# Optimization experiments

Hardware: AMD Instinct MI355X
Metric: run time of the kernel (lower is better)

The kernel has to match this reference:

```python
import jax, jax.numpy as jnp
import numpy as np

N = 50000       # nodes
E = 1_600_000   # edges (avg degree 32)
NFEAT = 256
NHID = 128
NCLASS = 128    # must equal NHID for the gated skip connection to type-check


def setup_inputs() -> dict:
    key = jax.random.key(0)
    ks = jax.random.split(key, 16)
    g = 0.02  # xavier gain used in the module
    inp = {
        "x": jax.random.normal(ks[0], (N, NFEAT), dtype=jnp.float32),
        "row": jax.random.randint(ks[1], (E,), 0, N, dtype=jnp.int32),
        "col": jax.random.randint(ks[2], (E,), 0, N, dtype=jnp.int32),
        # GatedSkipConnection params (shared across the three skip calls)
        "W_sc": jax.random.normal(ks[3], (NFEAT, NHID), dtype=jnp.float32) * 0.05,
        "W_ci": jax.random.normal(ks[4], (NHID, NHID), dtype=jnp.float32) * 0.05,
        "b_ci": jnp.zeros((NHID,), dtype=jnp.float32),
        "W_co": jax.random.normal(ks[5], (NHID, NHID), dtype=jnp.float32) * 0.05,
        "b_co": jnp.zeros((NHID,), dtype=jnp.float32),
        # GraphSAGE layer weights: [2*in, out], bias [1, out] (init to 0 per module)
        "W0": jax.random.normal(ks[6], (2 * NFEAT, NHID), dtype=jnp.float32) * g,
        "b0": jnp.zeros((1, NHID), dtype=jnp.float32),
        "W1": jax.random.normal(ks[7], (2 * NHID, NHID), dtype=jnp.float32) * g,
        "b1": jnp.zeros((1, NHID), dtype=jnp.float32),
        "W2": jax.random.normal(ks[8], (2 * NHID, NCLASS), dtype=jnp.float32) * g,
        "b2": jnp.zeros((1, NCLASS), dtype=jnp.float32),
        # fc0: Linear(nhid, nclass)
        "Wf": jax.random.normal(ks[9], (NHID, NCLASS), dtype=jnp.float32) * 0.05,
        "bf": jnp.zeros((NCLASS,), dtype=jnp.float32),
    }
    return inp


def _sage(x, row, col, inv_deg, W, b):
    # adj @ x : sum source features x[col] into destination rows `row`
    agg = jax.ops.segment_sum(x[col], row, num_segments=N)  # [N, d]
    agg = agg * inv_deg[:, None]                            # degree normalization
    support = jnp.concatenate([x, agg], axis=1)             # [N, 2d]
    return support @ W + b


def _gsc(in_x, out_x, W_sc, W_ci, b_ci, W_co, b_co):
    in_x = in_x @ W_sc if in_x.shape[1] != out_x.shape[1] else in_x
    z = jax.nn.sigmoid(in_x @ W_ci + b_ci + out_x @ W_co + b_co)
    return z * out_x + (1.0 - z) * in_x


def reference(x, row, col, W_sc, W_ci, b_ci, W_co, b_co,
              W0, b0, W1, b1, W2, b2, Wf, bf):
    deg = jax.ops.segment_sum(jnp.ones((E,), x.dtype), row, num_segments=N)
    inv_deg = 1.0 / jnp.maximum(deg, 1.0)  # guard isolated nodes

    residual = x
    o1 = _sage(x, row, col, inv_deg, W0, b0)
    o3 = jax.nn.relu(_gsc(residual, o1, W_sc, W_ci, b_ci, W_co, b_co))
    o4 = _sage(o3, row, col, inv_deg, W1, b1)
    o6 = jax.nn.relu(_gsc(residual, o4, W_sc, W_ci, b_ci, W_co, b_co))
    o7 = _sage(o6, row, col, inv_deg, W2, b2)
    o8 = _gsc(residual, o7, W_sc, W_ci, b_ci, W_co, b_co)
    return o8 @ Wf + bf
```

## Files before the change

### kernel.cpp

```cpp
#include <hip/hip_runtime.h>
#include <hip/hip_bf16.h>
#include <hip/hip_fp16.h>
#include <math.h>

#define NN 50000
#define EE 1600000
#define NFEAT 256
#define NHID 128
#define RNG 6250
#define NPASS 8

typedef _Float16 f16;
typedef _Float16 f16x8 __attribute__((ext_vector_type(8)));
typedef _Float16 f16x4 __attribute__((ext_vector_type(4)));
typedef float f32x4 __attribute__((ext_vector_type(4)));

__global__ void k_zero_i32(int* __restrict__ p, int n) {
    int i = blockIdx.x * 256 + threadIdx.x;
    if (i < n) p[i] = 0;
}

__global__ void k_slot(const int* __restrict__ row, int* __restrict__ cnt,
                       int* __restrict__ eslot, int e) {
    int i = blockIdx.x * 256 + threadIdx.x;
    if (i < e) eslot[i] = atomicAdd(&cnt[row[i]], 1);
}

__global__ void k_scan1(const int* __restrict__ deg, int* __restrict__ bsum, int n) {
    __shared__ int s[256];
    int t = threadIdx.x;
    int i = blockIdx.x * 256 + t;
    s[t] = (i < n) ? deg[i] : 0;
    __syncthreads();
    for (int off = 128; off > 0; off >>= 1) {
        if (t < off) s[t] += s[t + off];
        __syncthreads();
    }
    if (t == 0) bsum[blockIdx.x] = s[0];
}

__global__ void k_scan2(int* __restrict__ bsum, int nb) {
    if (blockIdx.x == 0 && threadIdx.x == 0) {
        int acc = 0;
        for (int i = 0; i < nb; ++i) { int t = bsum[i]; bsum[i] = acc; acc += t; }
    }
}

__global__ void k_scan3(const int* __restrict__ deg, const int* __restrict__ bsum,
                        int* __restrict__ rp, float* __restrict__ invd, int n) {
    __shared__ int buf[2][256];
    int t = threadIdx.x;
    int i = blockIdx.x * 256 + t;
    int v = (i < n) ? deg[i] : 0;
    buf[0][t] = v;
    __syncthreads();
    int sel = 0;
    for (int off = 1; off < 256; off <<= 1) {
        int x = buf[sel][t];
        if (t >= off) x += buf[sel][t - off];
        buf[sel ^ 1][t] = x;
        sel ^= 1;
        __syncthreads();
    }
    int incl = buf[sel][t];
    int excl = incl - v;
    if (i < n) {
        int base = bsum[blockIdx.x];
        rp[i] = base + excl;
        invd[i] = 1.0f / fmaxf((float)v, 1.0f);
        if (i == n - 1) rp[n] = base + incl;
    }
}

__global__ void k_fill8(const int* __restrict__ row, const int* __restrict__ col,
                        const int* __restrict__ eslot, const int* __restrict__ rp,
                        int* __restrict__ ci, int e) {
    int i = blockIdx.x * 256 + threadIdx.x;
    if (i >= e) return;
    int r = row[i];
    int lo = blockIdx.y * RNG;
    if (r >= lo && r < lo + RNG) ci[rp[r] + eslot[i]] = col[i];
}

__global__ void k_cvt_x(const float* __restrict__ src, f16* __restrict__ dst, int n4) {
    int i = blockIdx.x * 256 + threadIdx.x;
    if (i >= n4) return;
    float4 v = reinterpret_cast<const float4*>(src)[i];
    f16x4 h = {(f16)v.x, (f16)v.y, (f16)v.z, (f16)v.w};
    reinterpret_cast<f16x4*>(dst)[i] = h;
}

struct WD { const float* s; f16* d; int K; };
struct WDs { WD w[10]; };
__global__ void k_cvtW(WDs ds) {
    WD w = ds.w[blockIdx.y];
    int total = w.K * 128;
    for (int idx = blockIdx.x * 256 + threadIdx.x; idx < total; idx += gridDim.x * 256) {
        int k = idx >> 7, c = idx & 127;
        w.d[c * w.K + k] = (f16)w.s[idx];
    }
}

__global__ __launch_bounds__(256) void k_agg2h(const f16* __restrict__ P,
                                               const int* __restrict__ rp,
                                               const int* __restrict__ ci,
                                               const float* __restrict__ invd,
                                               const f16* __restrict__ T,
                                               f16* __restrict__ OUT, int n) {
    int node = blockIdx.x * 16 + (threadIdx.x >> 4);
    if (node >= n) return;
    int lane = threadIdx.x & 15;
    int s = rp[node], e = rp[node + 1];
    float acc[8];
#pragma unroll
    for (int q = 0; q < 8; ++q) acc[q] = 0.0f;
    int j = s;
    for (; j + 4 <= e; j += 4) {
        int n0 = ci[j], n1 = ci[j + 1], n2 = ci[j + 2], n3 = ci[j + 3];
        f16x8 v0 = *reinterpret_cast<const f16x8*>(P + (size_t)n0 * 128 + lane * 8);
        f16x8 v1 = *reinterpret_cast<const f16x8*>(P + (size_t)n1 * 128 + lane * 8);
        f16x8 v2 = *reinterpret_cast<const f16x8*>(P + (size_t)n2 * 128 + lane * 8);
        f16x8 v3 = *reinterpret_cast<const f16x8*>(P + (size_t)n3 * 128 + lane * 8);
#pragma unroll
        for (int q = 0; q < 8; ++q)
            acc[q] += ((float)v0[q] + (float)v1[q]) + ((float)v2[q] + (float)v3[q]);
    }
    for (; j < e; ++j) {
        f16x8 v0 = *reinterpret_cast<const f16x8*>(P + (size_t)ci[j] * 128 + lane * 8);
#pragma unroll
        for (int q = 0; q < 8; ++q) acc[q] += (float)v0[q];
    }
    float scl = invd[node];
    f16x8 tv = *reinterpret_cast<const f16x8*>(T + (size_t)node * 128 + lane * 8);
    f16x8 o;
#pragma unroll
    for (int q = 0; q < 8; ++q) o[q] = (f16)((float)tv[q] + scl * acc[q]);
    *reinterpret_cast<f16x8*>(OUT + (size_t)node * 128 + lane * 8) = o;
}

#define LDSSTR 40

__device__ __forceinline__ void stage_A(const f16* __restrict__ A, f16* sA,
                                        int row0, int K, int kb, int tid, int n) {
    int r = tid >> 2, ch = tid & 3;
    int gr = row0 + r;
    uint4 v = make_uint4(0, 0, 0, 0);
    if (gr < n) v = *reinterpret_cast<const uint4*>(A + (size_t)gr * K + kb + ch * 8);
    *reinterpret_cast<uint4*>(sA + r * LDSSTR + ch * 8) = v;
}

__device__ __forceinline__ void stage_B(const f16* __restrict__ Wt, f16* sB,
                                        int K, int kb, int tid) {
#pragma unroll
    for (int i = 0; i < 2; ++i) {
        int idx = tid + i * 256;
        int c = idx >> 2, ch = idx & 3;
        uint4 v = *reinterpret_cast<const uint4*>(Wt + (size_t)c * K + kb + ch * 8);
        *reinterpret_cast<uint4*>(sB + c * LDSSTR + ch * 8) = v;
    }
}

template <int K, int NW, bool F32OUT>
__global__ __launch_bounds__(256) void k_mgemm(const f16* __restrict__ A,
                                               const f16* __restrict__ Wt0,
                                               const f16* __restrict__ Wt1,
                                               const f16* __restrict__ Wt2,
                                               const float* __restrict__ bias0,
                                               void* __restrict__ C0,
                                               void* __restrict__ C1,
                                               void* __restrict__ C2, int n) {
    __shared__ f16 sA[64 * LDSSTR];
    __shared__ f16 sB[128 * LDSSTR];

    const f16* Wt = Wt0;
    const float* bias = bias0;
    void* C = C0;
    if (NW > 1 && blockIdx.y == 1) { Wt = Wt1; bias = nullptr; C = C1; }
    if (NW > 2 && blockIdx.y == 2) { Wt = Wt2; bias = nullptr; C = C2; }

    const int tid = threadIdx.x;
    const int row0 = blockIdx.x * 64;
    const int wid = tid >> 6, l = tid & 63;
    const int wr = wid >> 1, wc = wid & 1;
    const int lr = l & 15, lk = (l >> 4) * 8;

    f32x4 acc[2][4];
#pragma unroll
    for (int m = 0; m < 2; ++m)
#pragma unroll
        for (int q = 0; q < 4; ++q) acc[m][q] = (f32x4){0.f, 0.f, 0.f, 0.f};

    for (int kt = 0; kt < K / 32; ++kt) {
        stage_A(A, sA, row0, K, kt * 32, tid, n);
        stage_B(Wt, sB, K, kt * 32, tid);
        __syncthreads();
        f16x8 aF[2], bF[4];
#pragma unroll
        for (int m = 0; m < 2; ++m)
            aF[m] = *reinterpret_cast<f16x8*>(sA + (wr * 32 + m * 16 + lr) * LDSSTR + lk);
#pragma unroll
        for (int q = 0; q < 4; ++q)
            bF[q] = *reinterpret_cast<f16x8*>(sB + (wc * 64 + q * 16 + lr) * LDSSTR + lk);
#pragma unroll
        for (int m = 0; m < 2; ++m)
#pragma unroll
            for (int q = 0; q < 4; ++q)
                acc[m][q] = __builtin_amdgcn_mfma_f32_16x16x32_f16(aF[m], bF[q],
                                                                   acc[m][q], 0, 0, 0);
        __syncthreads();
    }

    const int lr4 = (l >> 4) * 4;
#pragma unroll
    for (int m = 0; m < 2; ++m)
#pragma unroll
        for (int q = 0; q < 4; ++q) {
            int c = wc * 64 + q * 16 + (l & 15);
            float b = bias ? bias[c] : 0.0f;
#pragma unroll
            for (int reg = 0; reg < 4; ++reg) {
                int r = row0 + wr * 32 + m * 16 + lr4 + reg;
                if (r >= n) continue;
                float v = acc[m][q][reg] + b;
                if (F32OUT) ((float*)C)[(size_t)r * 128 + c] = v;
                else        ((f16*)C)[(size_t)r * 128 + c] = (f16)v;
            }
        }
}

template <int RELU>
__global__ __launch_bounds__(256) void k_ggemm(const f16* __restrict__ Asc,
                                               const f16* __restrict__ At0,
                                               const f16* __restrict__ Wci,
                                               const f16* __restrict__ Wco,
                                               const float* __restrict__ bci,
                                               const float* __restrict__ bco,
                                               f16* __restrict__ C, int n) {
    __shared__ f16 sA[64 * LDSSTR];
    __shared__ f16 sB[128 * LDSSTR];

    const int tid = threadIdx.x;
    const int row0 = blockIdx.x * 64;
    const int wid = tid >> 6, l = tid & 63;
    const int wr = wid >> 1, wc = wid & 1;
    const int lr = l & 15, lk = (l >> 4) * 8;

    f32x4 acc[2][4];
#pragma unroll
    for (int m = 0; m < 2; ++m)
#pragma unroll
        for (int q = 0; q < 4; ++q) acc[m][q] = (f32x4){0.f, 0.f, 0.f, 0.f};

    for (int kt = 0; kt < 8; ++kt) {
        const f16* A = (kt < 4) ? Asc : At0;
        const f16* Wt = (kt < 4) ? Wci : Wco;
        int kb = (kt & 3) * 32;
        stage_A(A, sA, row0, 128, kb, tid, n);
        stage_B(Wt, sB, 128, kb, tid);
        __syncthreads();
        f16x8 aF[2], bF[4];
#pragma unroll
        for (int m = 0; m < 2; ++m)
            aF[m] = *reinterpret_cast<f16x8*>(sA + (wr * 32 + m * 16 + lr) * LDSSTR + lk);
#pragma unroll
        for (int q = 0; q < 4; ++q)
            bF[q] = *reinterpret_cast<f16x8*>(sB + (wc * 64 + q * 16 + lr) * LDSSTR + lk);
#pragma unroll
        for (int m = 0; m < 2; ++m)
#pragma unroll
            for (int q = 0; q < 4; ++q)
                acc[m][q] = __builtin_amdgcn_mfma_f32_16x16x32_f16(aF[m], bF[q],
                                                                   acc[m][q], 0, 0, 0);
        __syncthreads();
    }

    const int lr4 = (l >> 4) * 4;
#pragma unroll
    for (int m = 0; m < 2; ++m)
#pragma unroll
        for (int q = 0; q < 4; ++q) {
            int c = wc * 64 + q * 16 + (l & 15);
            float b = bci[c] + bco[c];
#pragma unroll
            for (int reg = 0; reg < 4; ++reg) {
                int r = row0 + wr * 32 + m * 16 + lr4 + reg;
                if (r >= n) continue;
                float v = acc[m][q][reg] + b;
                float z = 1.0f / (1.0f + __expf(-v));
                float o = (float)At0[(size_t)r * 128 + c];
                float s = (float)Asc[(size_t)r * 128 + c];
                float outv = z * o + (1.0f - z) * s;
                if (RELU) outv = fmaxf(outv, 0.0f);
                C[(size_t)r * 128 + c] = (f16)outv;
            }
        }
}

extern "C" void kernel_launch(void* const* d_in, const int* in_sizes, int n_in,
                              void* d_out, int out_size, void* d_ws, size_t ws_size,
                              hipStream_t stream) {
    const float* x    = (const float*)d_in[0];
    const int*   row  = (const int*)d_in[1];
    const int*   col  = (const int*)d_in[2];
    const float* W_sc = (const float*)d_in[3];
    const float* W_ci = (const float*)d_in[4];
    const float* b_ci = (const float*)d_in[5];
    const float* W_co = (const float*)d_in[6];
    const float* b_co = (const float*)d_in[7];
    const float* W0   = (const float*)d_in[8];
    const float* b0   = (const float*)d_in[9];
    const float* W1   = (const float*)d_in[10];
    const float* b1   = (const float*)d_in[11];
    const float* W2   = (const float*)d_in[12];
    const float* b2   = (const float*)d_in[13];
    const float* Wf   = (const float*)d_in[14];
    const float* bf   = (const float*)d_in[15];
    float* out = (float*)d_out;

    char* p = (char*)d_ws;
    auto alloc = [&](size_t bytes) {
        char* q = p;
        p += (bytes + 255) & ~(size_t)255;
        return q;
    };
    int*   cnt   = (int*)alloc(NN * 4);
    int*   rp    = (int*)alloc((NN + 1) * 4);
    int*   bsum  = (int*)alloc(256 * 4);
    float* invd  = (float*)alloc(NN * 4);
    int*   ci    = (int*)alloc(EE * 4);
    int*   eslot = (int*)alloc(EE * 4);
    f16*   x_h   = (f16*)alloc((size_t)NN * 256 * 2);
    f16*   sc_h  = (f16*)alloc((size_t)NN * 128 * 2);
    f16*   T_h   = (f16*)alloc((size_t)NN * 128 * 2);
    f16*   P_h   = (f16*)alloc((size_t)NN * 128 * 2);
    f16*   t0_h  = (f16*)alloc((size_t)NN * 128 * 2);
    f16*   t1_h  = (f16*)alloc((size_t)NN * 128 * 2);
    f16* W0t_t = (f16*)alloc(256 * 128 * 2);
    f16* W0b_t = (f16*)alloc(256 * 128 * 2);
    f16* Wsc_t = (f16*)alloc(256 * 128 * 2);
    f16* W1t_t = (f16*)alloc(128 * 128 * 2);
    f16* W1b_t = (f16*)alloc(128 * 128 * 2);
    f16* W2t_t = (f16*)alloc(128 * 128 * 2);
    f16* W2b_t = (f16*)alloc(128 * 128 * 2);
    f16* Wci_t = (f16*)alloc(128 * 128 * 2);
    f16* Wco_t = (f16*)alloc(128 * 128 * 2);
    f16* Wf_t  = (f16*)alloc(128 * 128 * 2);

    const int NB_N  = (NN + 255) / 256;
    const int NB_E  = (EE + 255) / 256;
    const int GB    = (NN + 63) / 64;
    const int AGG_B = (NN + 15) / 16;

    k_cvt_x<<<(NN * 256 / 4 + 255) / 256, 256, 0, stream>>>(x, x_h, NN * 256 / 4);
    WDs ds;
    ds.w[0] = {W0, W0t_t, 256};
    ds.w[1] = {W0 + 256 * 128, W0b_t, 256};
    ds.w[2] = {W_sc, Wsc_t, 256};
    ds.w[3] = {W1, W1t_t, 128};
    ds.w[4] = {W1 + 128 * 128, W1b_t, 128};
    ds.w[5] = {W2, W2t_t, 128};
    ds.w[6] = {W2 + 128 * 128, W2b_t, 128};
    ds.w[7] = {W_ci, Wci_t, 128};
    ds.w[8] = {W_co, Wco_t, 128};
    ds.w[9] = {Wf, Wf_t, 128};
    k_cvtW<<<dim3(64, 10), 256, 0, stream>>>(ds);

    k_zero_i32<<<NB_N, 256, 0, stream>>>(cnt, NN);
    k_slot<<<NB_E, 256, 0, stream>>>(row, cnt, eslot, EE);
    k_scan1<<<NB_N, 256, 0, stream>>>(cnt, bsum, NN);
    k_scan2<<<1, 1, 0, stream>>>(bsum, NB_N);
    k_scan3<<<NB_N, 256, 0, stream>>>(cnt, bsum, rp, invd, NN);
    k_fill8<<<dim3(NB_E, NPASS), 256, 0, stream>>>(row, col, eslot, rp, ci, EE);

    k_mgemm<256, 3, false><<<dim3(GB, 3), 256, 0, stream>>>(
        x_h, W0t_t, W0b_t, Wsc_t, b0, T_h, P_h, sc_h, NN);
    k_agg2h<<<AGG_B, 256, 0, stream>>>(P_h, rp, ci, invd, T_h, t0_h, NN);
    k_ggemm<1><<<GB, 256, 0, stream>>>(sc_h, t0_h, Wci_t, Wco_t,
                                       b_ci, b_co, t1_h, NN);

    k_mgemm<128, 2, false><<<dim3(GB, 2), 256, 0, stream>>>(
        t1_h, W1t_t, W1b_t, nullptr, b1, T_h, P_h, nullptr, NN);
    k_agg2h<<<AGG_B, 256, 0, stream>>>(P_h, rp, ci, invd, T_h, t0_h, NN);
    k_ggemm<1><<<GB, 256, 0, stream>>>(sc_h, t0_h, Wci_t, Wco_t,
                                       b_ci, b_co, t1_h, NN);

    k_mgemm<128, 2, false><<<dim3(GB, 2), 256, 0, stream>>>(
        t1_h, W2t_t, W2b_t, nullptr, b2, T_h, P_h, nullptr, NN);
    k_agg2h<<<AGG_B, 256, 0, stream>>>(P_h, rp, ci, invd, T_h, t0_h, NN);
    k_ggemm<0><<<GB, 256, 0, stream>>>(sc_h, t0_h, Wci_t, Wco_t,
                                       b_ci, b_co, t1_h, NN);

    k_mgemm<128, 1, true><<<GB, 256, 0, stream>>>(
        t1_h, Wf_t, nullptr, nullptr, bf, out, nullptr, nullptr, NN);
}
```

Baseline: 560.3 us.

## Merge prep kernels, pad degree counters, fold block scan, unroll gather by eight

Fuses the x conversion, counter zeroing and weight transposition into one launch, and folds the serial block-sum scan into the second scan kernel, so fewer kernels are launched. Degree counters are padded to 16 ints apart, which spreads the atomics across cache lines at the cost of a larger zeroing pass and strided scan reads. The aggregation loop now issues eight neighbor loads per iteration instead of four, giving more memory-level parallelism at the cost of extra registers.

```diff
diff --git a/kernel.cpp b/kernel.cpp
--- a/kernel.cpp
+++ b/kernel.cpp
@@ -9,28 +9,57 @@
 #define NHID 128
 #define RNG 6250
 #define NPASS 8
+#define CPAD 16
 
 typedef _Float16 f16;
 typedef _Float16 f16x8 __attribute__((ext_vector_type(8)));
 typedef _Float16 f16x4 __attribute__((ext_vector_type(4)));
 typedef float f32x4 __attribute__((ext_vector_type(4)));
 
-__global__ void k_zero_i32(int* __restrict__ p, int n) {
-    int i = blockIdx.x * 256 + threadIdx.x;
-    if (i < n) p[i] = 0;
+struct WPtrs {
+    const float* s[10];
+    f16* d[10];
+};
+
+__global__ __launch_bounds__(256) void k_prep(const float* __restrict__ x,
+                                              f16* __restrict__ xh, int n4,
+                                              int* __restrict__ cnt, int nz4,
+                                              WPtrs wp, int wtotal,
+                                              int zb0, int wb0, int wblocks) {
+    int b = blockIdx.x;
+    if (b < zb0) {
+        int i = b * 256 + threadIdx.x;
+        if (i < n4) {
+            float4 v = reinterpret_cast<const float4*>(x)[i];
+            f16x4 h = {(f16)v.x, (f16)v.y, (f16)v.z, (f16)v.w};
+            reinterpret_cast<f16x4*>(xh)[i] = h;
+        }
+    } else if (b < wb0) {
+        int i = (b - zb0) * 256 + threadIdx.x;
+        if (i < nz4) reinterpret_cast<int4*>(cnt)[i] = make_int4(0, 0, 0, 0);
+    } else {
+        for (int idx = (b - wb0) * 256 + threadIdx.x; idx < wtotal;
+             idx += wblocks * 256) {
+            int wsel, rem, K;
+            if (idx < 3 * 32768) { wsel = idx >> 15; rem = idx & 32767; K = 256; }
+            else { int t = idx - 3 * 32768; wsel = 3 + (t >> 14); rem = t & 16383; K = 128; }
+            int k = rem >> 7, c = rem & 127;
+            wp.d[wsel][c * K + k] = (f16)wp.s[wsel][rem];
+        }
+    }
 }
 
 __global__ void k_slot(const int* __restrict__ row, int* __restrict__ cnt,
                        int* __restrict__ eslot, int e) {
     int i = blockIdx.x * 256 + threadIdx.x;
-    if (i < e) eslot[i] = atomicAdd(&cnt[row[i]], 1);
-}
-
-__global__ void k_scan1(const int* __restrict__ deg, int* __restrict__ bsum, int n) {
+    if (i < e) eslot[i] = atomicAdd(&cnt[(size_t)row[i] * CPAD], 1);
+}
+
+__global__ void k_scan1(const int* __restrict__ cnt, int* __restrict__ bsum, int n) {
     __shared__ int s[256];
     int t = threadIdx.x;
     int i = blockIdx.x * 256 + t;
-    s[t] = (i < n) ? deg[i] : 0;
+    s[t] = (i < n) ? cnt[(size_t)i * CPAD] : 0;
     __syncthreads();
     for (int off = 128; off > 0; off >>= 1) {
         if (t < off) s[t] += s[t + off];
@@ -39,19 +68,27 @@
     if (t == 0) bsum[blockIdx.x] = s[0];
 }
 
-__global__ void k_scan2(int* __restrict__ bsum, int nb) {
-    if (blockIdx.x == 0 && threadIdx.x == 0) {
-        int acc = 0;
-        for (int i = 0; i < nb; ++i) { int t = bsum[i]; bsum[i] = acc; acc += t; }
-    }
-}
-
-__global__ void k_scan3(const int* __restrict__ deg, const int* __restrict__ bsum,
-                        int* __restrict__ rp, float* __restrict__ invd, int n) {
+__global__ void k_scan3(const int* __restrict__ cnt, const int* __restrict__ bsum,
+                        int* __restrict__ rp, float* __restrict__ invd,
+                        int n, int nb) {
     __shared__ int buf[2][256];
+    __shared__ int bpre[2][256];
     int t = threadIdx.x;
+
+    bpre[0][t] = (t < nb) ? bsum[t] : 0;
+    __syncthreads();
+    int bs = 0;
+    for (int off = 1; off < 256; off <<= 1) {
+        int v = bpre[bs][t];
+        if (t >= off) v += bpre[bs][t - off];
+        bpre[bs ^ 1][t] = v;
+        bs ^= 1;
+        __syncthreads();
+    }
+    int base = (blockIdx.x == 0) ? 0 : bpre[bs][blockIdx.x - 1];
+
     int i = blockIdx.x * 256 + t;
-    int v = (i < n) ? deg[i] : 0;
+    int v = (i < n) ? cnt[(size_t)i * CPAD] : 0;
     buf[0][t] = v;
     __syncthreads();
     int sel = 0;
@@ -65,7 +102,6 @@
     int incl = buf[sel][t];
     int excl = incl - v;
     if (i < n) {
-        int base = bsum[blockIdx.x];
         rp[i] = base + excl;
         invd[i] = 1.0f / fmaxf((float)v, 1.0f);
         if (i == n - 1) rp[n] = base + incl;
@@ -80,25 +116,6 @@
     int r = row[i];
     int lo = blockIdx.y * RNG;
     if (r >= lo && r < lo + RNG) ci[rp[r] + eslot[i]] = col[i];
-}
-
-__global__ void k_cvt_x(const float* __restrict__ src, f16* __restrict__ dst, int n4) {
-    int i = blockIdx.x * 256 + threadIdx.x;
-    if (i >= n4) return;
-    float4 v = reinterpret_cast<const float4*>(src)[i];
-    f16x4 h = {(f16)v.x, (f16)v.y, (f16)v.z, (f16)v.w};
-    reinterpret_cast<f16x4*>(dst)[i] = h;
-}
-
-struct WD { const float* s; f16* d; int K; };
-struct WDs { WD w[10]; };
-__global__ void k_cvtW(WDs ds) {
-    WD w = ds.w[blockIdx.y];
-    int total = w.K * 128;
-    for (int idx = blockIdx.x * 256 + threadIdx.x; idx < total; idx += gridDim.x * 256) {
-        int k = idx >> 7, c = idx & 127;
-        w.d[c * w.K + k] = (f16)w.s[idx];
-    }
 }
 
 __global__ __launch_bounds__(256) void k_agg2h(const f16* __restrict__ P,
@@ -115,15 +132,15 @@
 #pragma unroll
     for (int q = 0; q < 8; ++q) acc[q] = 0.0f;
     int j = s;
-    for (; j + 4 <= e; j += 4) {
-        int n0 = ci[j], n1 = ci[j + 1], n2 = ci[j + 2], n3 = ci[j + 3];
-        f16x8 v0 = *reinterpret_cast<const f16x8*>(P + (size_t)n0 * 128 + lane * 8);
-        f16x8 v1 = *reinterpret_cast<const f16x8*>(P + (size_t)n1 * 128 + lane * 8);
-        f16x8 v2 = *reinterpret_cast<const f16x8*>(P + (size_t)n2 * 128 + lane * 8);
-        f16x8 v3 = *reinterpret_cast<const f16x8*>(P + (size_t)n3 * 128 + lane * 8);
+    for (; j + 8 <= e; j += 8) {
+        f16x8 v[8];
+#pragma unroll
+        for (int u = 0; u < 8; ++u)
+            v[u] = *reinterpret_cast<const f16x8*>(P + (size_t)ci[j + u] * 128 + lane * 8);
 #pragma unroll
         for (int q = 0; q < 8; ++q)
-            acc[q] += ((float)v0[q] + (float)v1[q]) + ((float)v2[q] + (float)v3[q]);
+            acc[q] += (((float)v[0][q] + (float)v[1][q]) + ((float)v[2][q] + (float)v[3][q])) +
+                      (((float)v[4][q] + (float)v[5][q]) + ((float)v[6][q] + (float)v[7][q]));
     }
     for (; j < e; ++j) {
         f16x8 v0 = *reinterpret_cast<const f16x8*>(P + (size_t)ci[j] * 128 + lane * 8);
@@ -323,7 +340,7 @@
         p += (bytes + 255) & ~(size_t)255;
         return q;
     };
-    int*   cnt   = (int*)alloc(NN * 4);
+    int*   cnt   = (int*)alloc((size_t)NN * CPAD * 4);
     int*   rp    = (int*)alloc((NN + 1) * 4);
     int*   bsum  = (int*)alloc(256 * 4);
     float* invd  = (float*)alloc(NN * 4);
@@ -351,25 +368,29 @@
     const int GB    = (NN + 63) / 64;
     const int AGG_B = (NN + 15) / 16;
 
-    k_cvt_x<<<(NN * 256 / 4 + 255) / 256, 256, 0, stream>>>(x, x_h, NN * 256 / 4);
-    WDs ds;
-    ds.w[0] = {W0, W0t_t, 256};
-    ds.w[1] = {W0 + 256 * 128, W0b_t, 256};
-    ds.w[2] = {W_sc, Wsc_t, 256};
-    ds.w[3] = {W1, W1t_t, 128};
-    ds.w[4] = {W1 + 128 * 128, W1b_t, 128};
-    ds.w[5] = {W2, W2t_t, 128};
-    ds.w[6] = {W2 + 128 * 128, W2b_t, 128};
-    ds.w[7] = {W_ci, Wci_t, 128};
-    ds.w[8] = {W_co, Wco_t, 128};
-    ds.w[9] = {Wf, Wf_t, 128};
-    k_cvtW<<<dim3(64, 10), 256, 0, stream>>>(ds);
-
-    k_zero_i32<<<NB_N, 256, 0, stream>>>(cnt, NN);
+    const int N4   = NN * 256 / 4;
+    const int NZ4  = NN * CPAD / 4;
+    const int ZB0  = (N4 + 255) / 256;
+    const int WB0  = ZB0 + (NZ4 + 255) / 256;
+    const int WBLK = 84;
+    const int WTOT = 3 * 32768 + 7 * 16384;
+    WPtrs wp;
+    wp.s[0] = W0;             wp.d[0] = W0t_t;
+    wp.s[1] = W0 + 256 * 128; wp.d[1] = W0b_t;
+    wp.s[2] = W_sc;           wp.d[2] = Wsc_t;
+    wp.s[3] = W1;             wp.d[3] = W1t_t;
+    wp.s[4] = W1 + 128 * 128; wp.d[4] = W1b_t;
+    wp.s[5] = W2;             wp.d[5] = W2t_t;
+    wp.s[6] = W2 + 128 * 128; wp.d[6] = W2b_t;
+    wp.s[7] = W_ci;           wp.d[7] = Wci_t;
+    wp.s[8] = W_co;           wp.d[8] = Wco_t;
+    wp.s[9] = Wf;             wp.d[9] = Wf_t;
+    k_prep<<<WB0 + WBLK, 256, 0, stream>>>(x, x_h, N4, cnt, NZ4, wp, WTOT,
+                                           ZB0, WB0, WBLK);
+
     k_slot<<<NB_E, 256, 0, stream>>>(row, cnt, eslot, EE);
     k_scan1<<<NB_N, 256, 0, stream>>>(cnt, bsum, NN);
-    k_scan2<<<1, 1, 0, stream>>>(bsum, NB_N);
-    k_scan3<<<NB_N, 256, 0, stream>>>(cnt, bsum, rp, invd, NN);
+    k_scan3<<<NB_N, 256, 0, stream>>>(cnt, bsum, rp, invd, NN, NB_N);
     k_fill8<<<dim3(NB_E, NPASS), 256, 0, stream>>>(row, col, eslot, rp, ci, EE);
 
     k_mgemm<256, 3, false><<<dim3(GB, 3), 256, 0, stream>>>(
```

Measured after the change: 541.8 us. -3.3%, faster.
